# Kernel optimization log

Hardware: AMD Instinct MI355X
Metric: run time of the kernel (lower is better)

The kernel has to match this reference:

```python
import jax, jax.numpy as jnp
import numpy as np
from jax import lax

DN = ('NCHW', 'OIHW', 'NCHW')


def _conv(x, w):
    # Conv2d(k=3, stride=2, padding=1, bias=False)
    return lax.conv_general_dilated(x, w, (2, 2), [(1, 1), (1, 1)], dimension_numbers=DN)


def _deconv(x, w):
    # ConvTranspose2d(k=3, stride=2, padding=1, output_padding=1, bias=False)
    # == input dilation 2 with asymmetric pad (k-1-p, k-1-p+output_padding) = (1, 2)
    return lax.conv_general_dilated(x, w, (1, 1), [(1, 2), (1, 2)], lhs_dilation=(2, 2), dimension_numbers=DN)


def _vq(z, codebook):
    B, C, H, W = z.shape
    z_flat = jnp.transpose(z, (0, 2, 3, 1)).reshape(-1, C)  # [BHW, C]
    dist = (jnp.sum(z_flat * z_flat, axis=1, keepdims=True)
            - 2.0 * z_flat @ codebook.T
            + jnp.sum(codebook * codebook, axis=1)[None, :])  # [BHW, K]
    ids = jnp.argmin(dist, axis=1)  # [BHW]
    e_k = codebook[ids]  # [BHW, C]
    e_k_st = z_flat + lax.stop_gradient(e_k - z_flat)
    e_k = jnp.transpose(e_k.reshape(B, H, W, C), (0, 3, 1, 2))
    e_k_st = jnp.transpose(e_k_st.reshape(B, H, W, C), (0, 3, 1, 2))
    return e_k, e_k_st, ids.reshape(B, H, W)


def _forward(x, enc_w0, enc_w1, enc_w2, codebook, dec_w0, dec_w1, dec_w2):
    # encoder
    h = jax.nn.relu(_conv(x, enc_w0))
    h = jax.nn.relu(_conv(h, enc_w1))
    z = _conv(h, enc_w2)  # no relu on last encoder layer
    # vector quantize
    e_k, e_k_st, ids = _vq(z, codebook)
    # decoder
    d = jax.nn.relu(_deconv(e_k_st, dec_w0))
    d = jax.nn.relu(_deconv(d, dec_w1))
    out = jax.nn.sigmoid(_deconv(d, dec_w2))
    return out, z, e_k, ids


def setup_inputs() -> dict:
    key = jax.random.key(0)
    ks = jax.random.split(key, 8)
    fan = lambda s: 1.0 / np.sqrt(np.prod(s[1:]))
    K = 1024
    return {
        'x': jax.random.uniform(ks[0], (32, 3, 256, 256), dtype=jnp.float32),
        'enc_w0': jax.random.normal(ks[1], (64, 3, 3, 3), jnp.float32) * fan((64, 3, 3, 3)),
        'enc_w1': jax.random.normal(ks[2], (128, 64, 3, 3), jnp.float32) * fan((128, 64, 3, 3)),
        'enc_w2': jax.random.normal(ks[3], (256, 128, 3, 3), jnp.float32) * fan((256, 128, 3, 3)),
        'codebook': jax.random.uniform(ks[4], (K, 256), jnp.float32, -1.0 / K, 1.0 / K),
        'dec_w0': jax.random.normal(ks[5], (128, 256, 3, 3), jnp.float32) * fan((128, 256, 3, 3)),
        'dec_w1': jax.random.normal(ks[6], (64, 128, 3, 3), jnp.float32) * fan((64, 128, 3, 3)),
        'dec_w2': jax.random.normal(ks[7], (3, 64, 3, 3), jnp.float32) * fan((3, 64, 3, 3)),
    }


def reference(x, enc_w0, enc_w1, enc_w2, codebook, dec_w0, dec_w1, dec_w2):
    return _forward(x, enc_w0, enc_w1, enc_w2, codebook, dec_w0, dec_w1, dec_w2)
```

## Files before the change

### kernel.cpp

```cpp
#include <hip/hip_runtime.h>
#include <math.h>


__global__ __launch_bounds__(256) void pad_zero_k(float* __restrict__ buf,
                                                  int HP, int WP) {
  float* p = buf + (size_t)blockIdx.x * HP * WP;
  const int tid = threadIdx.x;
  if (tid < WP) p[tid] = 0.f;
  if (tid >= 1 && tid < HP) p[(size_t)tid * WP] = 0.f;
}

template <int CIN, int COB, int PY, int LX, int ACT>
__global__ __launch_bounds__(256) void conv3x3_s2_py(
    const float* __restrict__ in, const float* __restrict__ wgt,
    float* __restrict__ out, int COUT, int HIN, int WIN, int tilesW,
    int OHP, int OWP, int po) {
  const int HOUT = HIN >> 1, WOUT = WIN >> 1;
  const int YG = 256 / LX;
  const int tid = threadIdx.x;
  const int x = (blockIdx.x % tilesW) * LX + (tid % LX);
  const int y0 = (blockIdx.x / tilesW) * (YG * PY) + (tid / LX) * PY;
  const int co0 = blockIdx.y * COB;
  const int n = blockIdx.z;
  if (x >= WOUT || y0 >= HOUT) return;

  float acc[COB][PY], sum[COB][PY];
#pragma unroll
  for (int c = 0; c < COB; ++c)
#pragma unroll
    for (int r = 0; r < PY; ++r) { acc[c][r] = 0.f; sum[c][r] = 0.f; }

  const int ix0 = 2 * x - 1;
  const int iy0 = 2 * y0 - 1;
  for (int ci = 0; ci < CIN; ++ci) {
    const float* ip = in + (size_t)(n * CIN + ci) * HIN * WIN;
    float v[2 * PY + 1][3];
#pragma unroll
    for (int j = 0; j < 2 * PY + 1; ++j) {
      const int iy = iy0 + j;
      const bool yok = (unsigned)iy < (unsigned)HIN;
#pragma unroll
      for (int kx = 0; kx < 3; ++kx) {
        const int ix = ix0 + kx;
        v[j][kx] =
            (yok && (unsigned)ix < (unsigned)WIN) ? ip[iy * WIN + ix] : 0.f;
      }
    }
#pragma unroll
    for (int t = 0; t < 9; ++t) {
      const int kk = ci * 9 + t;
      if (CIN * 9 > 384 && (kk == 384 || kk == 768)) {
#pragma unroll
        for (int c = 0; c < COB; ++c)
#pragma unroll
          for (int r = 0; r < PY; ++r) {
            sum[c][r] = sum[c][r] + acc[c][r];
            acc[c][r] = 0.f;
          }
      }
      const int ky = t / 3, kx = t % 3;
#pragma unroll
      for (int c = 0; c < COB; ++c) {
        const float w = wgt[((size_t)(co0 + c) * CIN + ci) * 9 + t];
#pragma unroll
        for (int r = 0; r < PY; ++r)
          acc[c][r] = fmaf(v[2 * r + ky][kx], w, acc[c][r]);
      }
    }
  }
#pragma unroll
  for (int c = 0; c < COB; ++c)
#pragma unroll
    for (int r = 0; r < PY; ++r) {
      if (y0 + r < HOUT) {
        float rv = sum[c][r] + acc[c][r];
        if (ACT == 1) rv = fmaxf(rv, 0.f);
        out[(((size_t)n * COUT + co0 + c) * OHP + y0 + r + po) * OWP + x + po] =
            rv;
      }
    }
}

template <int CIN, int COB, int PY, int LX, int WINL, int ACT, int PO>
__global__ __launch_bounds__(256) void conv3x3_s2_pad(
    const float* __restrict__ in, const float* __restrict__ wgt,
    float* __restrict__ out, int COUT, int tilesW) {
  constexpr int WP = WINL + 1;
  constexpr int HP = WINL + 1;
  constexpr size_t planeP = (size_t)HP * WP;
  constexpr int HOUT = WINL >> 1, WOUT = WINL >> 1;
  constexpr int OWP = WOUT + PO;
  constexpr int OHP = HOUT + PO;
  const int YG = 256 / LX;
  const int tid = threadIdx.x;
  const int x = (blockIdx.x % tilesW) * LX + (tid % LX);
  const int y0 = (blockIdx.x / tilesW) * (YG * PY) + (tid / LX) * PY;
  const int co0 = blockIdx.y * COB;
  const int n = blockIdx.z;
  if (x >= WOUT || y0 >= HOUT) return;

  float acc[COB][PY], sum[COB][PY];
#pragma unroll
  for (int c = 0; c < COB; ++c)
#pragma unroll
    for (int r = 0; r < PY; ++r) { acc[c][r] = 0.f; sum[c][r] = 0.f; }

  const float* bp = in + (size_t)(n * CIN) * planeP + (size_t)(2 * y0) * WP +
                    2 * x;
  for (int ci = 0; ci < CIN; ++ci, bp += planeP) {
    float v[2 * PY + 1][3];
#pragma unroll
    for (int j = 0; j < 2 * PY + 1; ++j)
#pragma unroll
      for (int kx = 0; kx < 3; ++kx) v[j][kx] = bp[j * WP + kx];
#pragma unroll
    for (int t = 0; t < 9; ++t) {
      const int kk = ci * 9 + t;
      if (CIN * 9 > 384 && (kk == 384 || kk == 768)) {
#pragma unroll
        for (int c = 0; c < COB; ++c)
#pragma unroll
          for (int r = 0; r < PY; ++r) {
            sum[c][r] = sum[c][r] + acc[c][r];
            acc[c][r] = 0.f;
          }
      }
      const int ky = t / 3, kx = t % 3;
#pragma unroll
      for (int c = 0; c < COB; ++c) {
        const float w = wgt[((size_t)(co0 + c) * CIN + ci) * 9 + t];
#pragma unroll
        for (int r = 0; r < PY; ++r)
          acc[c][r] = fmaf(v[2 * r + ky][kx], w, acc[c][r]);
      }
    }
  }
#pragma unroll
  for (int c = 0; c < COB; ++c)
#pragma unroll
    for (int r = 0; r < PY; ++r) {
      float rv = sum[c][r] + acc[c][r];
      if (ACT == 1) rv = fmaxf(rv, 0.f);
      out[(((size_t)n * COUT + co0 + c) * OHP + y0 + r + PO) * OWP + x + PO] =
          rv;
    }
}

template <int CIN, int COB, int ACT>
__global__ __launch_bounds__(256) void deconv3x3_s2_quad2(
    const float* __restrict__ in, const float* __restrict__ wgt,
    float* __restrict__ out, int COUT, int HIN, int WIN, int tilesW) {
  const int HOUT = HIN * 2, WOUT = WIN * 2;
  const int tid = threadIdx.x;
  const int mx0 = ((blockIdx.x % tilesW) * 16 + (tid & 15)) * 2;
  const int my = (blockIdx.x / tilesW) * 16 + (tid >> 4);
  const int co0 = blockIdx.y * COB;
  const int n = blockIdx.z;
  if (mx0 >= WIN || my >= HIN) return;
  const bool xe = (mx0 + 2 < WIN);
  const bool ye = (my + 1 < HIN);

  float accA[COB][4], accB[COB][4];
#pragma unroll
  for (int c = 0; c < COB; ++c)
#pragma unroll
    for (int q = 0; q < 4; ++q) { accA[c][q] = 0.f; accB[c][q] = 0.f; }

  const size_t plane = (size_t)HIN * WIN;
  const float* ip = in + (size_t)(n * CIN) * plane + (size_t)my * WIN + mx0;
  for (int ci = 0; ci < CIN; ++ci, ip += plane) {
    const float v00 = ip[0];
    const float v01 = ip[1];
    const float v02 = xe ? ip[2] : 0.f;
    const float v10 = ye ? ip[WIN] : 0.f;
    const float v11 = ye ? ip[WIN + 1] : 0.f;
    const float v12 = (xe && ye) ? ip[WIN + 2] : 0.f;
#pragma unroll
    for (int c = 0; c < COB; ++c) {
      const float* w = wgt + ((size_t)(co0 + c) * CIN + ci) * 9;
      accA[c][0] = fmaf(v00, w[4], accA[c][0]);
      accA[c][1] = fmaf(v00, w[3], accA[c][1]);
      accA[c][1] = fmaf(v01, w[5], accA[c][1]);
      accA[c][2] = fmaf(v00, w[1], accA[c][2]);
      accA[c][2] = fmaf(v10, w[7], accA[c][2]);
      accA[c][3] = fmaf(v00, w[0], accA[c][3]);
      accA[c][3] = fmaf(v01, w[2], accA[c][3]);
      accA[c][3] = fmaf(v10, w[6], accA[c][3]);
      accA[c][3] = fmaf(v11, w[8], accA[c][3]);
      accB[c][0] = fmaf(v01, w[4], accB[c][0]);
      accB[c][1] = fmaf(v01, w[3], accB[c][1]);
      accB[c][1] = fmaf(v02, w[5], accB[c][1]);
      accB[c][2] = fmaf(v01, w[1], accB[c][2]);
      accB[c][2] = fmaf(v11, w[7], accB[c][2]);
      accB[c][3] = fmaf(v01, w[0], accB[c][3]);
      accB[c][3] = fmaf(v02, w[2], accB[c][3]);
      accB[c][3] = fmaf(v11, w[6], accB[c][3]);
      accB[c][3] = fmaf(v12, w[8], accB[c][3]);
    }
  }

  const int y0 = 2 * my, x0 = 2 * mx0;
#pragma unroll
  for (int c = 0; c < COB; ++c) {
    float rA[4], rB[4];
#pragma unroll
    for (int q = 0; q < 4; ++q) {
      float a = accA[c][q], b = accB[c][q];
      if (ACT == 1) { a = fmaxf(a, 0.f); b = fmaxf(b, 0.f); }
      if (ACT == 2) {
        a = 1.f / (1.f + expf(-a));
        b = 1.f / (1.f + expf(-b));
      }
      rA[q] = a; rB[q] = b;
    }
    float* op = out + (((size_t)n * COUT + co0 + c) * HOUT + y0) * WOUT + x0;
    float4 lo; lo.x = rA[0]; lo.y = rA[1]; lo.z = rB[0]; lo.w = rB[1];
    float4 hi; hi.x = rA[2]; hi.y = rA[3]; hi.z = rB[2]; hi.w = rB[3];
    *reinterpret_cast<float4*>(op) = lo;
    *reinterpret_cast<float4*>(op + WOUT) = hi;
  }
}

__global__ __launch_bounds__(256) void z2_np_k(const float* __restrict__ z,
                                               float* __restrict__ z2) {
#pragma clang fp contract(off)
  const int p = blockIdx.x * 256 + threadIdx.x;
  const int n = p >> 10, hw = p & 1023;
  const float* zb = z + (size_t)n * 262144 + hw;
  float blk[2];
#pragma unroll
  for (int b = 0; b < 2; ++b) {
    float r[8];
#pragma unroll
    for (int j = 0; j < 8; ++j) {
      const float v = zb[(size_t)(b * 128 + j) * 1024];
      r[j] = v * v;
    }
    for (int i = 8; i < 128; i += 8) {
#pragma unroll
      for (int j = 0; j < 8; ++j) {
        const float v = zb[(size_t)(b * 128 + i + j) * 1024];
        const float m = v * v;
        r[j] = r[j] + m;
      }
    }
    blk[b] = ((r[0] + r[1]) + (r[2] + r[3])) + ((r[4] + r[5]) + (r[6] + r[7]));
  }
  z2[p] = blk[0] + blk[1];
}

__global__ __launch_bounds__(256) void c2_np_k(const float* __restrict__ cb,
                                               float* __restrict__ c2) {
#pragma clang fp contract(off)
  const int jrow = blockIdx.x * 256 + threadIdx.x;
  const float* row = cb + (size_t)jrow * 256;
  float blk[2];
#pragma unroll
  for (int b = 0; b < 2; ++b) {
    float r[8];
#pragma unroll
    for (int j = 0; j < 8; ++j) {
      const float v = row[b * 128 + j];
      r[j] = v * v;
    }
    for (int i = 8; i < 128; i += 8) {
#pragma unroll
      for (int j = 0; j < 8; ++j) {
        const float v = row[b * 128 + i + j];
        const float m = v * v;
        r[j] = r[j] + m;
      }
    }
    blk[b] = ((r[0] + r[1]) + (r[2] + r[3])) + ((r[4] + r[5]) + (r[6] + r[7]));
  }
  c2[jrow] = blk[0] + blk[1];
}

__global__ __launch_bounds__(256) void vq_scores_f32_k(
    const float* __restrict__ z, const float* __restrict__ cb,
    const float* __restrict__ z2, const float* __restrict__ c2,
    int* __restrict__ bestid) {
  __shared__ float zS[32][64];
  __shared__ float cS[64][33];
  const int tid = threadIdx.x;
  const int p0 = blockIdx.x * 64;
  const int n = p0 >> 10;
  const int hw0 = p0 & 1023;
  const float* zb = z + (size_t)n * 262144 + hw0;

  const int tp = tid >> 4;
  const int tj = tid & 15;

  float z2v[4];
#pragma unroll
  for (int ii = 0; ii < 4; ++ii) z2v[ii] = z2[p0 + tp * 4 + ii];

  float run_d[4];
  int run_id[4];
#pragma unroll
  for (int ii = 0; ii < 4; ++ii) { run_d[ii] = 3.4e38f; run_id[ii] = 0; }

  for (int j0 = 0; j0 < 1024; j0 += 64) {
    float acc[4][4];
#pragma unroll
    for (int a = 0; a < 4; ++a)
#pragma unroll
      for (int b = 0; b < 4; ++b) acc[a][b] = 0.f;

    for (int k0 = 0; k0 < 256; k0 += 32) {
      __syncthreads();
#pragma unroll
      for (int i = 0; i < 8; ++i) {
        const int q = i * 256 + tid;
        const int zc = q >> 6, zl = q & 63;
        zS[zc][zl] = zb[(size_t)(k0 + zc) * 1024 + zl];
        const int cj = q >> 5, cd = q & 31;
        cS[cj][cd] = cb[(size_t)(j0 + cj) * 256 + k0 + cd];
      }
      __syncthreads();
#pragma unroll
      for (int d = 0; d < 32; ++d) {
        const float za = zS[d][tp * 4 + 0];
        const float zbv = zS[d][tp * 4 + 1];
        const float zc = zS[d][tp * 4 + 2];
        const float zd = zS[d][tp * 4 + 3];
        const float c0 = cS[0 * 16 + tj][d];
        const float c1 = cS[1 * 16 + tj][d];
        const float c2v = cS[2 * 16 + tj][d];
        const float c3 = cS[3 * 16 + tj][d];
        acc[0][0] = fmaf(za, c0, acc[0][0]);
        acc[0][1] = fmaf(za, c1, acc[0][1]);
        acc[0][2] = fmaf(za, c2v, acc[0][2]);
        acc[0][3] = fmaf(za, c3, acc[0][3]);
        acc[1][0] = fmaf(zbv, c0, acc[1][0]);
        acc[1][1] = fmaf(zbv, c1, acc[1][1]);
        acc[1][2] = fmaf(zbv, c2v, acc[1][2]);
        acc[1][3] = fmaf(zbv, c3, acc[1][3]);
        acc[2][0] = fmaf(zc, c0, acc[2][0]);
        acc[2][1] = fmaf(zc, c1, acc[2][1]);
        acc[2][2] = fmaf(zc, c2v, acc[2][2]);
        acc[2][3] = fmaf(zc, c3, acc[2][3]);
        acc[3][0] = fmaf(zd, c0, acc[3][0]);
        acc[3][1] = fmaf(zd, c1, acc[3][1]);
        acc[3][2] = fmaf(zd, c2v, acc[3][2]);
        acc[3][3] = fmaf(zd, c3, acc[3][3]);
      }
    }

    {
#pragma clang fp contract(off)
#pragma unroll
      for (int ii = 0; ii < 4; ++ii) {
#pragma unroll
        for (int jj = 0; jj < 4; ++jj) {
          const int j = j0 + jj * 16 + tj;
          const float m2 = 2.0f * acc[ii][jj];
          const float t1 = z2v[ii] + c2[j];
          const float dist = t1 - m2;
          if (dist < run_d[ii] || (dist == run_d[ii] && j < run_id[ii])) {
            run_d[ii] = dist;
            run_id[ii] = j;
          }
        }
      }
    }
  }

#pragma unroll
  for (int m = 1; m < 16; m <<= 1) {
#pragma unroll
    for (int ii = 0; ii < 4; ++ii) {
      const float od = __shfl_xor(run_d[ii], m, 64);
      const int oid = __shfl_xor(run_id[ii], m, 64);
      if (od < run_d[ii] || (od == run_d[ii] && oid < run_id[ii])) {
        run_d[ii] = od;
        run_id[ii] = oid;
      }
    }
  }
  if (tj == 0) {
#pragma unroll
    for (int ii = 0; ii < 4; ++ii) bestid[p0 + tp * 4 + ii] = run_id[ii];
  }
}

__global__ __launch_bounds__(256) void vq_gather_k(
    const int* __restrict__ bestid, const float* __restrict__ cb,
    float* __restrict__ ek, float* __restrict__ ids) {
  const int p = blockIdx.x * 256 + threadIdx.x;
  const int id = bestid[p];
  ids[p] = (float)id;
  const int n = p >> 10, hw = p & 1023;
  float* ekb = ek + (size_t)n * 262144 + hw;
  const float* cbr = cb + (size_t)id * 256;
  for (int c = 0; c < 256; ++c) ekb[(size_t)c * 1024] = cbr[c];
}

extern "C" void kernel_launch(void* const* d_in, const int* in_sizes, int n_in,
                              void* d_out, int out_size, void* d_ws,
                              size_t ws_size, hipStream_t stream) {
  const float* x = (const float*)d_in[0];
  const float* enc_w0 = (const float*)d_in[1];
  const float* enc_w1 = (const float*)d_in[2];
  const float* enc_w2 = (const float*)d_in[3];
  const float* codebook = (const float*)d_in[4];
  const float* dec_w0 = (const float*)d_in[5];
  const float* dec_w1 = (const float*)d_in[6];
  const float* dec_w2 = (const float*)d_in[7];

  float* out = (float*)d_out;
  float* z_out = out + 6291456;
  float* ek_out = z_out + 8388608;
  float* ids_out = ek_out + 8388608;

  float* ws = (float*)d_ws;
  float* h1p = ws;
  float* h2p = ws + 34080768;
  float* d1 = h2p;
  float* d2 = h1p;
  float* s = ws + 51386368;
  float* z2 = s;
  float* c2 = s + 32768;
  int* bestid = (int*)(s + 33792);

  pad_zero_k<<<32 * 64, 256, 0, stream>>>(h1p, 129, 129);
  pad_zero_k<<<32 * 128, 256, 0, stream>>>(h2p, 65, 65);

  conv3x3_s2_py<3, 8, 4, 16, 1><<<dim3(16, 8, 32), 256, 0, stream>>>(
      x, enc_w0, h1p, 64, 256, 256, 8, 129, 129, 1);
  conv3x3_s2_pad<64, 8, 4, 16, 128, 1, 1><<<dim3(4, 16, 32), 256, 0, stream>>>(
      h1p, enc_w1, h2p, 128, 4);
  conv3x3_s2_pad<128, 8, 4, 32, 64, 0, 0><<<dim3(1, 32, 32), 256, 0, stream>>>(
      h2p, enc_w2, z_out, 256, 1);

  z2_np_k<<<128, 256, 0, stream>>>(z_out, z2);
  c2_np_k<<<4, 256, 0, stream>>>(codebook, c2);
  vq_scores_f32_k<<<512, 256, 0, stream>>>(z_out, codebook, z2, c2, bestid);
  vq_gather_k<<<128, 256, 0, stream>>>(bestid, codebook, ek_out, ids_out);

  deconv3x3_s2_quad2<256, 8, 1><<<dim3(2, 16, 32), 256, 0, stream>>>(
      ek_out, dec_w0, d1, 128, 32, 32, 1);
  deconv3x3_s2_quad2<128, 8, 1><<<dim3(8, 8, 32), 256, 0, stream>>>(
      d1, dec_w1, d2, 64, 64, 64, 2);
  deconv3x3_s2_quad2<64, 3, 2><<<dim3(32, 1, 32), 256, 0, stream>>>(
      d2, dec_w2, out, 3, 128, 128, 4);
}
```

Baseline: 1.704 ms.

## Split VQ codebook search across two block halves and vectorize shared loads

The VQ distance kernel now splits the 1024-entry codebook into two halves along a second grid dimension, doubling block count from 512 to 1024. Each half writes partial minimum distances and ids, which the gather kernel merges with the same tie-breaking. The codebook tile is also stored transposed in shared memory so each thread reads its four codebook values and its four z values with float4 loads. Codebook columns per thread become contiguous, and c2 and z2 are read as float4. The cost is extra partial-result traffic and a small reduction step.

```diff
diff --git a/kernel.cpp b/kernel.cpp
--- a/kernel.cpp
+++ b/kernel.cpp
@@ -276,14 +276,15 @@
   c2[jrow] = blk[0] + blk[1];
 }
 
-__global__ __launch_bounds__(256) void vq_scores_f32_k(
+__global__ __launch_bounds__(256) void vq_scores_part_k(
     const float* __restrict__ z, const float* __restrict__ cb,
     const float* __restrict__ z2, const float* __restrict__ c2,
-    int* __restrict__ bestid) {
+    float* __restrict__ pdist, int* __restrict__ pid) {
   __shared__ float zS[32][64];
-  __shared__ float cS[64][33];
+  __shared__ float cT[32][68];
   const int tid = threadIdx.x;
   const int p0 = blockIdx.x * 64;
+  const int jb = blockIdx.y;
   const int n = p0 >> 10;
   const int hw0 = p0 & 1023;
   const float* zb = z + (size_t)n * 262144 + hw0;
@@ -291,16 +292,16 @@
   const int tp = tid >> 4;
   const int tj = tid & 15;
 
-  float z2v[4];
-#pragma unroll
-  for (int ii = 0; ii < 4; ++ii) z2v[ii] = z2[p0 + tp * 4 + ii];
+  const float4 z2q =
+      *reinterpret_cast<const float4*>(&z2[p0 + tp * 4]);
+  const float z2v[4] = {z2q.x, z2q.y, z2q.z, z2q.w};
 
   float run_d[4];
   int run_id[4];
 #pragma unroll
   for (int ii = 0; ii < 4; ++ii) { run_d[ii] = 3.4e38f; run_id[ii] = 0; }
 
-  for (int j0 = 0; j0 < 1024; j0 += 64) {
+  for (int j0 = jb * 512; j0 < jb * 512 + 512; j0 += 64) {
     float acc[4][4];
 #pragma unroll
     for (int a = 0; a < 4; ++a)
@@ -314,48 +315,45 @@
         const int q = i * 256 + tid;
         const int zc = q >> 6, zl = q & 63;
         zS[zc][zl] = zb[(size_t)(k0 + zc) * 1024 + zl];
-        const int cj = q >> 5, cd = q & 31;
-        cS[cj][cd] = cb[(size_t)(j0 + cj) * 256 + k0 + cd];
+        const int cw = q >> 5, cd = q & 31;
+        cT[cd][cw] = cb[(size_t)(j0 + cw) * 256 + k0 + cd];
       }
       __syncthreads();
 #pragma unroll
       for (int d = 0; d < 32; ++d) {
-        const float za = zS[d][tp * 4 + 0];
-        const float zbv = zS[d][tp * 4 + 1];
-        const float zc = zS[d][tp * 4 + 2];
-        const float zd = zS[d][tp * 4 + 3];
-        const float c0 = cS[0 * 16 + tj][d];
-        const float c1 = cS[1 * 16 + tj][d];
-        const float c2v = cS[2 * 16 + tj][d];
-        const float c3 = cS[3 * 16 + tj][d];
-        acc[0][0] = fmaf(za, c0, acc[0][0]);
-        acc[0][1] = fmaf(za, c1, acc[0][1]);
-        acc[0][2] = fmaf(za, c2v, acc[0][2]);
-        acc[0][3] = fmaf(za, c3, acc[0][3]);
-        acc[1][0] = fmaf(zbv, c0, acc[1][0]);
-        acc[1][1] = fmaf(zbv, c1, acc[1][1]);
-        acc[1][2] = fmaf(zbv, c2v, acc[1][2]);
-        acc[1][3] = fmaf(zbv, c3, acc[1][3]);
-        acc[2][0] = fmaf(zc, c0, acc[2][0]);
-        acc[2][1] = fmaf(zc, c1, acc[2][1]);
-        acc[2][2] = fmaf(zc, c2v, acc[2][2]);
-        acc[2][3] = fmaf(zc, c3, acc[2][3]);
-        acc[3][0] = fmaf(zd, c0, acc[3][0]);
-        acc[3][1] = fmaf(zd, c1, acc[3][1]);
-        acc[3][2] = fmaf(zd, c2v, acc[3][2]);
-        acc[3][3] = fmaf(zd, c3, acc[3][3]);
+        const float4 zv = *reinterpret_cast<const float4*>(&zS[d][tp * 4]);
+        const float4 cv = *reinterpret_cast<const float4*>(&cT[d][tj * 4]);
+        acc[0][0] = fmaf(zv.x, cv.x, acc[0][0]);
+        acc[0][1] = fmaf(zv.x, cv.y, acc[0][1]);
+        acc[0][2] = fmaf(zv.x, cv.z, acc[0][2]);
+        acc[0][3] = fmaf(zv.x, cv.w, acc[0][3]);
+        acc[1][0] = fmaf(zv.y, cv.x, acc[1][0]);
+        acc[1][1] = fmaf(zv.y, cv.y, acc[1][1]);
+        acc[1][2] = fmaf(zv.y, cv.z, acc[1][2]);
+        acc[1][3] = fmaf(zv.y, cv.w, acc[1][3]);
+        acc[2][0] = fmaf(zv.z, cv.x, acc[2][0]);
+        acc[2][1] = fmaf(zv.z, cv.y, acc[2][1]);
+        acc[2][2] = fmaf(zv.z, cv.z, acc[2][2]);
+        acc[2][3] = fmaf(zv.z, cv.w, acc[2][3]);
+        acc[3][0] = fmaf(zv.w, cv.x, acc[3][0]);
+        acc[3][1] = fmaf(zv.w, cv.y, acc[3][1]);
+        acc[3][2] = fmaf(zv.w, cv.z, acc[3][2]);
+        acc[3][3] = fmaf(zv.w, cv.w, acc[3][3]);
       }
     }
 
     {
 #pragma clang fp contract(off)
+      const float4 c2q =
+          *reinterpret_cast<const float4*>(&c2[j0 + tj * 4]);
+      const float c2a[4] = {c2q.x, c2q.y, c2q.z, c2q.w};
 #pragma unroll
       for (int ii = 0; ii < 4; ++ii) {
 #pragma unroll
         for (int jj = 0; jj < 4; ++jj) {
-          const int j = j0 + jj * 16 + tj;
+          const int j = j0 + tj * 4 + jj;
           const float m2 = 2.0f * acc[ii][jj];
-          const float t1 = z2v[ii] + c2[j];
+          const float t1 = z2v[ii] + c2a[jj];
           const float dist = t1 - m2;
           if (dist < run_d[ii] || (dist == run_d[ii] && j < run_id[ii])) {
             run_d[ii] = dist;
@@ -380,19 +378,29 @@
   }
   if (tj == 0) {
 #pragma unroll
-    for (int ii = 0; ii < 4; ++ii) bestid[p0 + tp * 4 + ii] = run_id[ii];
-  }
-}
-
-__global__ __launch_bounds__(256) void vq_gather_k(
-    const int* __restrict__ bestid, const float* __restrict__ cb,
-    float* __restrict__ ek, float* __restrict__ ids) {
+    for (int ii = 0; ii < 4; ++ii) {
+      pdist[jb * 32768 + p0 + tp * 4 + ii] = run_d[ii];
+      pid[jb * 32768 + p0 + tp * 4 + ii] = run_id[ii];
+    }
+  }
+}
+
+__global__ __launch_bounds__(256) void vq_reduce_gather_k(
+    const float* __restrict__ pdist, const int* __restrict__ pid,
+    const float* __restrict__ cb, float* __restrict__ ek,
+    float* __restrict__ ids) {
   const int p = blockIdx.x * 256 + threadIdx.x;
-  const int id = bestid[p];
-  ids[p] = (float)id;
+  float bd = pdist[p];
+  int bi = pid[p];
+  {
+    const float od = pdist[32768 + p];
+    const int oi = pid[32768 + p];
+    if (od < bd || (od == bd && oi < bi)) { bd = od; bi = oi; }
+  }
+  ids[p] = (float)bi;
   const int n = p >> 10, hw = p & 1023;
   float* ekb = ek + (size_t)n * 262144 + hw;
-  const float* cbr = cb + (size_t)id * 256;
+  const float* cbr = cb + (size_t)bi * 256;
   for (int c = 0; c < 256; ++c) ekb[(size_t)c * 1024] = cbr[c];
 }
 
@@ -421,7 +429,8 @@
   float* s = ws + 51386368;
   float* z2 = s;
   float* c2 = s + 32768;
-  int* bestid = (int*)(s + 33792);
+  float* pdist = s + 33792;
+  int* pid = (int*)(s + 99328);
 
   pad_zero_k<<<32 * 64, 256, 0, stream>>>(h1p, 129, 129);
   pad_zero_k<<<32 * 128, 256, 0, stream>>>(h2p, 65, 65);
@@ -435,8 +444,10 @@
 
   z2_np_k<<<128, 256, 0, stream>>>(z_out, z2);
   c2_np_k<<<4, 256, 0, stream>>>(codebook, c2);
-  vq_scores_f32_k<<<512, 256, 0, stream>>>(z_out, codebook, z2, c2, bestid);
-  vq_gather_k<<<128, 256, 0, stream>>>(bestid, codebook, ek_out, ids_out);
+  vq_scores_part_k<<<dim3(512, 2), 256, 0, stream>>>(z_out, codebook, z2, c2,
+                                                     pdist, pid);
+  vq_reduce_gather_k<<<128, 256, 0, stream>>>(pdist, pid, codebook, ek_out,
+                                              ids_out);
 
   deconv3x3_s2_quad2<256, 8, 1><<<dim3(2, 16, 32), 256, 0, stream>>>(
       ek_out, dec_w0, d1, 128, 32, 32, 1);
```

After: 1.630 ms. 4.4% less time.
